# Kernel optimization log

Measured on AMD Instinct MI355X. Metric: run time of the kernel, lower is better.

Reference implementation:

```python
import jax, jax.numpy as jnp
import numpy as np

# dims: B=8, T=12, N=512, F_in=64, H=8, F'=out_features//H=8
NEG_SLOPE = 0.01  # torch LeakyReLU default


def setup_inputs() -> dict:
    key = jax.random.key(0)
    ks = jax.random.split(key, 8)
    B, T, N, Fin, H, Fp = 8, 12, 512, 64, 8, 8
    x = jax.random.normal(ks[0], (B, T, N, Fin), dtype=jnp.float32)
    # sparse-ish adjacency with guaranteed self loops (avoids all -inf rows)
    adj = (jax.random.uniform(ks[1], (N, N)) < 0.05).astype(jnp.float32)
    adj = jnp.clip(adj + jnp.eye(N, dtype=jnp.float32), 0.0, 1.0)
    # per-head Linear(in_features, F'): stacked weights [H, Fin, F'] + bias [H, F']
    W = jax.random.normal(ks[2], (H, Fin, Fp), dtype=jnp.float32) * 0.1
    Wb = jax.random.normal(ks[3], (H, Fp), dtype=jnp.float32) * 0.1
    # per-head Linear(2F', 1): split into src-half a1 (multiplies h_j, first F'
    # of the concat) and dst-half a2 (multiplies h_i), plus scalar bias ab
    a1 = jax.random.normal(ks[4], (H, Fp), dtype=jnp.float32) * 0.1
    a2 = jax.random.normal(ks[5], (H, Fp), dtype=jnp.float32) * 0.1
    ab = jax.random.normal(ks[6], (H,), dtype=jnp.float32) * 0.1
    return {"x": x, "adj": adj, "W": W, "Wb": Wb, "a1": a1, "a2": a2, "ab": ab}


def reference(x, adj, W, Wb, a1, a2, ab):
    # h[b,t,h,n,f'] = x @ W_h + b_h
    h = jnp.einsum('btni,hio->bthno', x, W) + Wb[:, None, :]
    # a(cat(h_j, h_i)) = a1.h_j + a2.h_i + ab  (exact decomposition of the
    # original broadcast-concat; avoids the O(N^2 * 2F') a_input tensor)
    s_src = jnp.einsum('bthno,ho->bthn', h, a1)  # contributes along j axis
    s_dst = jnp.einsum('bthno,ho->bthn', h, a2)  # contributes along i axis
    e = jax.nn.leaky_relu(
        s_src[..., None, :] + s_dst[..., :, None] + ab[:, None, None],
        negative_slope=NEG_SLOPE,
    )  # [B,T,H,N,N]
    e = jnp.where(adj == 0, -jnp.inf, e)
    attn = jax.nn.softmax(e, axis=-1)  # (dropout is identity in eval mode)
    h_prime = jnp.einsum('bthij,bthjo->bthio', attn, h)  # [B,T,H,N,F']
    B, T, H, N, Fp = h_prime.shape
    # concat heads along feature dim, matching torch.cat(head_outputs, -1)
    return h_prime.transpose(0, 1, 3, 2, 4).reshape(B, T, N, H * Fp)
```

## Files before the change

### kernel.cpp

```cpp
#include <hip/hip_runtime.h>
#include <math.h>

namespace {

constexpr int kN    = 512;
constexpr int kFin  = 64;
constexpr int kH    = 8;
constexpr int kFp   = 8;
constexpr int kBT   = 96;
constexpr int kNT   = 256;
constexpr int kMaxDeg = 104;
constexpr float kNeg = 0.01f;
constexpr float kL2E = 1.44269504088896340736f;

typedef _Float16 half8t __attribute__((ext_vector_type(8)));
typedef unsigned int uint;

__device__ __forceinline__ float fast_exp2(float v) {
#if __has_builtin(__builtin_amdgcn_exp2f)
  return __builtin_amdgcn_exp2f(v);
#else
  return exp2f(v);
#endif
}

constexpr int kOffBits = 0;
constexpr int kOffPerm = kOffBits + kN * 16;
constexpr int kOffDeg  = kOffPerm + kN;
constexpr int kOffIdx  = kOffDeg + kN;

__global__ void pack_adj_kernel(const float* __restrict__ adj,
                                uint* __restrict__ bitsR) {
  const int t = blockIdx.x * blockDim.x + threadIdx.x;
  const unsigned long long m = __ballot(adj[t] != 0.0f);
  const int lane = threadIdx.x & 63;
  if ((lane & 31) == 0) {
    const int i = t >> 9;
    const int w = (t & 511) >> 5;
    bitsR[i * 16 + w] = (uint)(m >> (lane & 32));
  }
}

__global__ __launch_bounds__(512) void csr_build_kernel(
    const uint* __restrict__ bitsR, uint* __restrict__ permG,
    uint* __restrict__ degG, uint* __restrict__ idxG) {
  __shared__ int base[128];
  const int i = threadIdx.x;

  uint b[16];
  int deg = 0;
#pragma unroll
  for (int w = 0; w < 16; ++w) {
    b[w] = bitsR[i * 16 + w];
    deg += __popc(b[w]);
  }
  const int dc = min(deg, 127);

  if (i < 128) base[i] = 0;
  __syncthreads();
  atomicAdd(&base[dc], 1);
  __syncthreads();
  if (i == 0) {
    int run = 0;
    for (int k = 0; k < 128; ++k) {
      const int c = base[k];
      base[k] = run;
      run += c;
    }
  }
  __syncthreads();
  const int pos = atomicAdd(&base[dc], 1);
  permG[pos] = (uint)i;
  degG[pos] = (uint)deg;

  int slot = 0;
#pragma unroll 1
  for (int w = 0; w < 16; ++w) {
    uint m = b[w];
    while (m) {
      const int j = w * 32 + __builtin_ctz(m);
      m &= m - 1;
      if (slot < kMaxDeg) idxG[slot * kN + pos] = (uint)j;
      ++slot;
    }
  }
  for (; slot < kMaxDeg; ++slot) idxG[slot * kN + pos] = 0u;
}

__global__ __launch_bounds__(kNT) void gat_sparse_kernel(
    const float* __restrict__ x, const uint* __restrict__ permG,
    const uint* __restrict__ degG, const uint* __restrict__ idxG,
    const float* __restrict__ W, const float* __restrict__ Wb,
    const float* __restrict__ a1, const float* __restrict__ a2,
    const float* __restrict__ ab, float* __restrict__ out) {
  __shared__ _Float16 h16S[kN * 8];
  __shared__ float ssrcS[kN];
  __shared__ float sdstS[kN];

  const int bt  = blockIdx.x >> 3;
  const int h   = blockIdx.x & 7;
  const int tid = threadIdx.x;

  const float* xb = x + (size_t)bt * kN * kFin;
  const float* Wl = W + h * kFin * kFp;

  float xr0[kFin], xr1[kFin];
  {
    const float4* p0 = reinterpret_cast<const float4*>(xb + (size_t)tid * kFin);
    const float4* p1 =
        reinterpret_cast<const float4*>(xb + (size_t)(tid + kNT) * kFin);
#pragma unroll
    for (int c4 = 0; c4 < kFin / 4; ++c4) {
      *reinterpret_cast<float4*>(&xr0[c4 * 4]) = p0[c4];
      *reinterpret_cast<float4*>(&xr1[c4 * 4]) = p1[c4];
    }
  }

  float acc0[kFp], acc1[kFp];
#pragma unroll
  for (int f = 0; f < kFp; ++f) {
    const float b = Wb[h * kFp + f];
    acc0[f] = b;
    acc1[f] = b;
  }
#pragma unroll
  for (int i = 0; i < kFin; ++i) {
#pragma unroll
    for (int f = 0; f < kFp; ++f) {
      const float wv = Wl[i * kFp + f];
      acc0[f] = fmaf(xr0[i], wv, acc0[f]);
      acc1[f] = fmaf(xr1[i], wv, acc1[f]);
    }
  }

  float s1a = 0.f, s2a = 0.f, s1b = 0.f, s2b = 0.f;
#pragma unroll
  for (int f = 0; f < kFp; ++f) {
    const float A1 = a1[h * kFp + f];
    const float A2 = a2[h * kFp + f];
    s1a = fmaf(acc0[f], A1, s1a);
    s2a = fmaf(acc0[f], A2, s2a);
    s1b = fmaf(acc1[f], A1, s1b);
    s2b = fmaf(acc1[f], A2, s2b);
  }
  const float abh = ab[h];
  ssrcS[tid]       = s1a * kL2E;
  ssrcS[tid + kNT] = s1b * kL2E;
  sdstS[tid]       = (s2a + abh) * kL2E;
  sdstS[tid + kNT] = (s2b + abh) * kL2E;

  {
    half8t hv;
#pragma unroll
    for (int f = 0; f < kFp; ++f) hv[f] = (_Float16)acc0[f];
    *reinterpret_cast<half8t*>(&h16S[(size_t)tid * 8]) = hv;
#pragma unroll
    for (int f = 0; f < kFp; ++f) hv[f] = (_Float16)acc1[f];
    *reinterpret_cast<half8t*>(&h16S[(size_t)(tid + kNT) * 8]) = hv;
  }
  __syncthreads();

  const int p0 = 2 * tid;
  const uint2 ip = *reinterpret_cast<const uint2*>(&permG[p0]);
  const uint2 dp = *reinterpret_cast<const uint2*>(&degG[p0]);
  const int i0 = (int)ip.x, i1 = (int)ip.y;
  const int d0 = (int)dp.x, d1 = (int)dp.y;
  const float sd0 = sdstS[i0];
  const float sd1 = sdstS[i1];
  const int dmax = max(d0, d1);

  float o0[kFp], o1[kFp];
#pragma unroll
  for (int f = 0; f < kFp; ++f) {
    o0[f] = 0.f;
    o1[f] = 0.f;
  }
  float sum0 = 0.f, sum1 = 0.f;

  uint2 jj = *reinterpret_cast<const uint2*>(&idxG[p0]);
#pragma unroll 1
  for (int slot = 0; slot < dmax; ++slot) {
    const int sn = min(slot + 1, kMaxDeg - 1);
    const uint2 jn = *reinterpret_cast<const uint2*>(&idxG[sn * kN + p0]);

    const half8t hv0 =
        *reinterpret_cast<const half8t*>(&h16S[(size_t)jj.x * 8]);
    const half8t hv1 =
        *reinterpret_cast<const half8t*>(&h16S[(size_t)jj.y * 8]);
    float e0 = ssrcS[jj.x] + sd0;
    float e1 = ssrcS[jj.y] + sd1;
    e0 = fmaxf(e0, e0 * kNeg);
    e1 = fmaxf(e1, e1 * kNeg);
    float q0 = fast_exp2(e0);
    float q1 = fast_exp2(e1);
    q0 = (slot < d0) ? q0 : 0.f;
    q1 = (slot < d1) ? q1 : 0.f;
    sum0 += q0;
    sum1 += q1;
#pragma unroll
    for (int f = 0; f < kFp; ++f) {
      o0[f] = fmaf((float)hv0[f], q0, o0[f]);
      o1[f] = fmaf((float)hv1[f], q1, o1[f]);
    }
    jj = jn;
  }

  const float r0 = 1.0f / sum0;
  const float r1 = 1.0f / sum1;
  float* q0p = out + (((size_t)bt * kN + i0) * kH + h) * kFp;
  float* q1p = out + (((size_t)bt * kN + i1) * kH + h) * kFp;
  reinterpret_cast<float4*>(q0p)[0] =
      make_float4(o0[0] * r0, o0[1] * r0, o0[2] * r0, o0[3] * r0);
  reinterpret_cast<float4*>(q0p)[1] =
      make_float4(o0[4] * r0, o0[5] * r0, o0[6] * r0, o0[7] * r0);
  reinterpret_cast<float4*>(q1p)[0] =
      make_float4(o1[0] * r1, o1[1] * r1, o1[2] * r1, o1[3] * r1);
  reinterpret_cast<float4*>(q1p)[1] =
      make_float4(o1[4] * r1, o1[5] * r1, o1[6] * r1, o1[7] * r1);
}

}

extern "C" void kernel_launch(void* const* d_in, const int* in_sizes, int n_in,
                              void* d_out, int out_size, void* d_ws, size_t ws_size,
                              hipStream_t stream) {
  const float* x   = (const float*)d_in[0];
  const float* adj = (const float*)d_in[1];
  const float* W   = (const float*)d_in[2];
  const float* Wb  = (const float*)d_in[3];
  const float* a1  = (const float*)d_in[4];
  const float* a2  = (const float*)d_in[5];
  const float* ab  = (const float*)d_in[6];
  float* out = (float*)d_out;

  uint* ws    = (uint*)d_ws;
  uint* bitsR = ws + kOffBits;
  uint* permG = ws + kOffPerm;
  uint* degG  = ws + kOffDeg;
  uint* idxG  = ws + kOffIdx;

  hipLaunchKernelGGL(pack_adj_kernel, dim3(kN * kN / kNT), dim3(kNT), 0, stream,
                     adj, bitsR);
  hipLaunchKernelGGL(csr_build_kernel, dim3(1), dim3(512), 0, stream,
                     bitsR, permG, degG, idxG);
  hipLaunchKernelGGL(gat_sparse_kernel, dim3(kBT * kH), dim3(kNT), 0, stream,
                     x, permG, degG, idxG, W, Wb, a1, a2, ab, out);
}
```

Before: 129.0 us.

## Parallelize CSR index fill across blocks and drop padding writes

```diff
diff --git a/kernel.cpp b/kernel.cpp
--- a/kernel.cpp
+++ b/kernel.cpp
@@ -27,7 +27,8 @@
 constexpr int kOffBits = 0;
 constexpr int kOffPerm = kOffBits + kN * 16;
 constexpr int kOffDeg  = kOffPerm + kN;
-constexpr int kOffIdx  = kOffDeg + kN;
+constexpr int kOffRPos = kOffDeg + kN;
+constexpr int kOffIdx  = kOffRPos + kN;
 
 __global__ void pack_adj_kernel(const float* __restrict__ adj,
                                 uint* __restrict__ bitsR) {
@@ -41,19 +42,14 @@
   }
 }
 
-__global__ __launch_bounds__(512) void csr_build_kernel(
+__global__ __launch_bounds__(512) void sort_assign_kernel(
     const uint* __restrict__ bitsR, uint* __restrict__ permG,
-    uint* __restrict__ degG, uint* __restrict__ idxG) {
+    uint* __restrict__ degG, uint* __restrict__ rowpos) {
   __shared__ int base[128];
   const int i = threadIdx.x;
-
-  uint b[16];
   int deg = 0;
 #pragma unroll
-  for (int w = 0; w < 16; ++w) {
-    b[w] = bitsR[i * 16 + w];
-    deg += __popc(b[w]);
-  }
+  for (int w = 0; w < 16; ++w) deg += __popc(bitsR[i * 16 + w]);
   const int dc = min(deg, 127);
 
   if (i < 128) base[i] = 0;
@@ -72,19 +68,30 @@
   const int pos = atomicAdd(&base[dc], 1);
   permG[pos] = (uint)i;
   degG[pos] = (uint)deg;
-
-  int slot = 0;
-#pragma unroll 1
-  for (int w = 0; w < 16; ++w) {
-    uint m = b[w];
-    while (m) {
-      const int j = w * 32 + __builtin_ctz(m);
-      m &= m - 1;
-      if (slot < kMaxDeg) idxG[slot * kN + pos] = (uint)j;
-      ++slot;
-    }
-  }
-  for (; slot < kMaxDeg; ++slot) idxG[slot * kN + pos] = 0u;
+  rowpos[i] = (uint)pos;
+}
+
+__global__ __launch_bounds__(64) void csr_fill_kernel(
+    const uint* __restrict__ bitsR, const uint* __restrict__ rowpos,
+    uint* __restrict__ idxG) {
+  const int i = blockIdx.x;
+  const int l = threadIdx.x;
+  const int pos = (int)rowpos[i];
+  uint b = (l < 16) ? bitsR[i * 16 + l] : 0u;
+  const int cnt = __popc(b);
+  int scan = cnt;
+#pragma unroll
+  for (int off = 1; off < 16; off <<= 1) {
+    const int v = __shfl_up(scan, off, 64);
+    if (l >= off) scan += v;
+  }
+  int slot = scan - cnt;
+  while (b) {
+    const int j = l * 32 + __builtin_ctz(b);
+    b &= b - 1;
+    idxG[slot * kN + pos] = (uint)j;
+    ++slot;
+  }
 }
 
 __global__ __launch_bounds__(kNT) void gat_sparse_kernel(
@@ -97,8 +104,8 @@
   __shared__ float ssrcS[kN];
   __shared__ float sdstS[kN];
 
-  const int bt  = blockIdx.x >> 3;
-  const int h   = blockIdx.x & 7;
+  const int bt  = blockIdx.x % kBT;
+  const int h   = blockIdx.x / kBT;
   const int tid = threadIdx.x;
 
   const float* xb = x + (size_t)bt * kN * kFin;
@@ -180,15 +187,15 @@
   uint2 jj = *reinterpret_cast<const uint2*>(&idxG[p0]);
 #pragma unroll 1
   for (int slot = 0; slot < dmax; ++slot) {
-    const int sn = min(slot + 1, kMaxDeg - 1);
-    const uint2 jn = *reinterpret_cast<const uint2*>(&idxG[sn * kN + p0]);
-
-    const half8t hv0 =
-        *reinterpret_cast<const half8t*>(&h16S[(size_t)jj.x * 8]);
-    const half8t hv1 =
-        *reinterpret_cast<const half8t*>(&h16S[(size_t)jj.y * 8]);
-    float e0 = ssrcS[jj.x] + sd0;
-    float e1 = ssrcS[jj.y] + sd1;
+    const uint2 jn =
+        *reinterpret_cast<const uint2*>(&idxG[(slot + 1) * kN + p0]);
+    const int j0 = (int)(jj.x & 511u);
+    const int j1 = (int)(jj.y & 511u);
+
+    const half8t hv0 = *reinterpret_cast<const half8t*>(&h16S[(size_t)j0 * 8]);
+    const half8t hv1 = *reinterpret_cast<const half8t*>(&h16S[(size_t)j1 * 8]);
+    float e0 = ssrcS[j0] + sd0;
+    float e1 = ssrcS[j1] + sd1;
     e0 = fmaxf(e0, e0 * kNeg);
     e1 = fmaxf(e1, e1 * kNeg);
     float q0 = fast_exp2(e0);
@@ -233,16 +240,19 @@
   const float* ab  = (const float*)d_in[6];
   float* out = (float*)d_out;
 
-  uint* ws    = (uint*)d_ws;
-  uint* bitsR = ws + kOffBits;
-  uint* permG = ws + kOffPerm;
-  uint* degG  = ws + kOffDeg;
-  uint* idxG  = ws + kOffIdx;
+  uint* ws     = (uint*)d_ws;
+  uint* bitsR  = ws + kOffBits;
+  uint* permG  = ws + kOffPerm;
+  uint* degG   = ws + kOffDeg;
+  uint* rowpos = ws + kOffRPos;
+  uint* idxG   = ws + kOffIdx;
 
   hipLaunchKernelGGL(pack_adj_kernel, dim3(kN * kN / kNT), dim3(kNT), 0, stream,
                      adj, bitsR);
-  hipLaunchKernelGGL(csr_build_kernel, dim3(1), dim3(512), 0, stream,
-                     bitsR, permG, degG, idxG);
+  hipLaunchKernelGGL(sort_assign_kernel, dim3(1), dim3(512), 0, stream,
+                     bitsR, permG, degG, rowpos);
+  hipLaunchKernelGGL(csr_fill_kernel, dim3(kN), dim3(64), 0, stream,
+                     bitsR, rowpos, idxG);
   hipLaunchKernelGGL(gat_sparse_kernel, dim3(kBT * kH), dim3(kNT), 0, stream,
                      x, permG, degG, idxG, W, Wb, a1, a2, ab, out);
 }
```

Result: faster. 107.7 us (-16.5%).
